# Performance work log

Measured on AMD Instinct MI355X. Metric: run time of the kernel, lower is better.

The kernel has to match this reference:

```python
import jax, jax.numpy as jnp
import numpy as np

H1, W1 = 16, 16  # SparseAttBlock stride
EPS = 1e-5       # BatchNorm eps


def _att(x, wx, bx, wy, by, wo, bo, gamma, beta):
    """DotProductAttBlock: 1x1 q/k projections, full softmax attention over
    the H*W tokens of each (small) block, then 1x1 conv + BatchNorm(train) + ReLU."""
    B, C, H, W = x.shape
    xf = x.reshape(B, C, H * W)                                  # [B,C,N]
    theta = jnp.einsum('mc,bcn->bnm', wx, xf) + bx               # [B,N,fmid]
    psi = jnp.einsum('mc,bcn->bmn', wy, xf) + by[:, None]        # [B,fmid,N]
    alpha = jax.nn.softmax(jnp.einsum('bnm,bmk->bnk', theta, psi), axis=2)  # [B,N,N]
    agg = jnp.einsum('bnk,bck->bcn', alpha, xf)                  # [B,C,N]
    out = jnp.einsum('oc,bcn->bon', wo, agg) + bo[:, None]       # [B,fout,N]
    # BatchNorm2d in training mode: biased batch stats over (batch, spatial)
    mean = out.mean(axis=(0, 2), keepdims=True)
    var = ((out - mean) ** 2).mean(axis=(0, 2), keepdims=True)
    out = (out - mean) * jax.lax.rsqrt(var + EPS) * gamma[:, None] + beta[:, None]
    return jax.nn.relu(out).reshape(B, -1, H, W)


def _forward(x, p1, p2):
    B, C, H, W = x.shape
    h2, w2 = H // H1, W // W1
    # pass 1: attention within each (H1,W1) block, blocks folded into batch
    xb = x.reshape(B, C, H1, h2, W1, w2).transpose(0, 3, 5, 1, 2, 4)
    xb = xb.reshape(B * h2 * w2, C, H1, W1)
    xb = _att(xb, *p1)
    # pass 2: attention across the (h2,w2) block grid
    xb = xb.reshape(B, h2, w2, C, H1, W1).transpose(0, 4, 5, 3, 1, 2)
    xb = xb.reshape(B * H1 * W1, C, h2, w2)
    xb = _att(xb, *p2)
    return xb.reshape(B, H1, W1, C, h2, w2).transpose(0, 3, 1, 4, 2, 5).reshape(B, C, H, W)


def setup_inputs() -> dict:
    key = jax.random.key(0)
    ks = jax.random.split(key, 20)
    B, C, FMID, H, W = 4, 128, 64, 256, 256
    s = 0.05
    d = {'x': jax.random.normal(ks[0], (B, C, H, W), jnp.float32)}
    d['w1x'] = jax.random.normal(ks[1], (FMID, C), jnp.float32) * s
    d['b1x'] = jax.random.normal(ks[2], (FMID,), jnp.float32) * s
    d['w1y'] = jax.random.normal(ks[3], (FMID, C), jnp.float32) * s
    d['b1y'] = jax.random.normal(ks[4], (FMID,), jnp.float32) * s
    d['w1o'] = jax.random.normal(ks[5], (C, C), jnp.float32) * s
    d['b1o'] = jax.random.normal(ks[6], (C,), jnp.float32) * s
    d['g1'] = jnp.ones((C,), jnp.float32)
    d['be1'] = jnp.zeros((C,), jnp.float32)
    d['w2x'] = jax.random.normal(ks[7], (FMID, C), jnp.float32) * s
    d['b2x'] = jax.random.normal(ks[8], (FMID,), jnp.float32) * s
    d['w2y'] = jax.random.normal(ks[9], (FMID, C), jnp.float32) * s
    d['b2y'] = jax.random.normal(ks[10], (FMID,), jnp.float32) * s
    d['w2o'] = jax.random.normal(ks[11], (C, C), jnp.float32) * s
    d['b2o'] = jax.random.normal(ks[12], (C,), jnp.float32) * s
    d['g2'] = jnp.ones((C,), jnp.float32)
    d['be2'] = jnp.zeros((C,), jnp.float32)
    return d


def reference(x, w1x, b1x, w1y, b1y, w1o, b1o, g1, be1,
              w2x, b2x, w2y, b2y, w2o, b2o, g2, be2):
    p1 = (w1x, b1x, w1y, b1y, w1o, b1o, g1, be1)
    p2 = (w2x, b2x, w2y, b2y, w2o, b2o, g2, be2)
    return _forward(x, p1, p2)
```

## Files before the change

### kernel.cpp

```cpp
#include <hip/hip_runtime.h>

typedef _Float16 f16;
typedef f16 f16x2 __attribute__((ext_vector_type(2)));
typedef f16 f16x4 __attribute__((ext_vector_type(4)));
typedef f16 f16x8 __attribute__((ext_vector_type(8)));
typedef float f32x4 __attribute__((ext_vector_type(4)));
typedef float f32x16 __attribute__((ext_vector_type(16)));
typedef unsigned int u32;
typedef u32 u32x2 __attribute__((ext_vector_type(2)));
typedef u32 u32x4 __attribute__((ext_vector_type(4)));

#define MFMA32(a, b, c) __builtin_amdgcn_mfma_f32_32x32x16_f16((a), (b), (c), 0, 0, 0)

__device__ __forceinline__ u32 pk2(float a, float b) {
    return __builtin_bit_cast(u32, __builtin_amdgcn_cvt_pkrtz(a, b));
}
__device__ __forceinline__ f16x4 lo4(f16x8 v) { return __builtin_shufflevector(v, v, 0, 1, 2, 3); }
__device__ __forceinline__ f16x4 hi4(f16x8 v) { return __builtin_shufflevector(v, v, 4, 5, 6, 7); }

__device__ __forceinline__ f16x8 xfrm(f32x16 v, int rb) {
    u32 a0 = pk2(v[rb + 0], v[rb + 1]);
    u32 a1 = pk2(v[rb + 2], v[rb + 3]);
    u32 b0 = pk2(v[rb + 4], v[rb + 5]);
    u32 b1 = pk2(v[rb + 6], v[rb + 7]);
    u32x2 r0 = __builtin_amdgcn_permlane32_swap(a0, b0, false, false);
    u32x2 r1 = __builtin_amdgcn_permlane32_swap(a1, b1, false, false);
    u32x4 aw = {r0.x, r1.x, r0.y, r1.y};
    return __builtin_bit_cast(f16x8, aw);
}
__device__ __forceinline__ f16x8 add8(f16x8 a, f16x8 b) {
    f16x8 r;
#pragma unroll
    for (int j = 0; j < 8; ++j) r[j] = a[j] + b[j];
    return r;
}

#define OFF_Y   65536
#define OFF_SST 98304
#define LDS_ATT 99328

#define WSTRIDE 32896

__global__ __launch_bounds__(512) void repack_kernel(const float* __restrict__ x,
                                                     f16* __restrict__ Xall) {
    __shared__ f16 XT[128 * 264];
    const int tid = threadIdx.x, g = blockIdx.x;
    const int b = g >> 8, i1 = (g >> 4) & 15, i2 = g & 15;
    const int h = i1 * 16 + i2;
    {
        const int c = tid >> 2, wq = (tid & 3) * 64;
        const float* src = x + (((size_t)b * 128 + c) * 256 + h) * 256 + wq;
        f16* dst = XT + c * 264 + wq;
#pragma unroll
        for (int i = 0; i < 16; ++i) {
            f32x4 v = *(const f32x4*)(src + i * 4);
            f16x4 o = {(f16)v[0], (f16)v[1], (f16)v[2], (f16)v[3]};
            *(f16x4*)(dst + i * 4) = o;
        }
    }
    __syncthreads();
    {
        const int w = tid >> 1, ch = (tid & 1) * 64;
        const int j1 = w >> 4, j2 = w & 15;
        f16* dst = Xall + (((size_t)b * 256 + i2 * 16 + j2) * 256 + i1 * 16 + j1) * 128 + ch;
#pragma unroll
        for (int i = 0; i < 8; ++i) {
            f16x8 v;
#pragma unroll
            for (int j = 0; j < 8; ++j) v[j] = XT[(ch + i * 8 + j) * 264 + w];
            *(f16x8*)(dst + i * 8) = v;
        }
    }
}

__global__ void wconv_kernel(const float* __restrict__ w1x, const float* __restrict__ w1y,
                             const float* __restrict__ w1o, const float* __restrict__ b1x,
                             const float* __restrict__ b1y, const float* __restrict__ w2x,
                             const float* __restrict__ w2y, const float* __restrict__ w2o,
                             const float* __restrict__ b2x, const float* __restrict__ b2y,
                             f16* __restrict__ Wf) {
    int i = blockIdx.x * 256 + threadIdx.x;
    if (i < 65536) {
        int p = i >> 15, idx = i & 32767;
        int j = idx & 7, lane = (idx >> 3) & 63, ks = (idx >> 9) & 7, r = idx >> 12;
        int row = r * 32 + (lane & 31);
        int c = ks * 16 + (lane >> 5) * 8 + j;
        const float* s;
        if (p == 0) s = (row < 128) ? w1o + row * 128 : (row < 192) ? w1x + (row - 128) * 128
                                                                   : w1y + (row - 192) * 128;
        else        s = (row < 128) ? w2o + row * 128 : (row < 192) ? w2x + (row - 128) * 128
                                                                   : w2y + (row - 192) * 128;
        Wf[p * WSTRIDE + idx] = (f16)s[c];
    } else {
        int idx2 = i - 65536;
        int p = idx2 >> 7, r = idx2 & 127;
        const float* bsrc = (p == 0) ? ((r < 64) ? b1x : b1y) : ((r < 64) ? b2x : b2y);
        Wf[p * WSTRIDE + 32768 + r] = (f16)bsrc[r & 63];
    }
}

template <int PASS>
__global__ __launch_bounds__(512, 2) void att_kernel(
    const f16* __restrict__ Xin, const f16* __restrict__ Wf, const float* __restrict__ bo,
    const float* __restrict__ bnab, f16* __restrict__ Uout, float* __restrict__ gstats,
    int t_stride, int s_stride) {
    __shared__ __align__(16) char smem[LDS_ATT];
    float* SST = (float*)(smem + OFF_SST);
    const int tid = threadIdx.x;
    const int w = tid >> 6, l = tid & 63, hl = l >> 5, l31 = l & 31;
    const int g = blockIdx.x, R0 = w * 32;

    if (tid < 256) SST[tid] = 0.f;

#pragma unroll
    for (int j = 0; j < 8; ++j) {
        int byte = (j * 512 + tid) * 16;
        *(f16x8*)(smem + byte) = *(const f16x8*)((const char*)Wf + byte);
    }

    const f16* src = Xin + (size_t)g * 32768 + (R0 + l31) * 128 + hl * 8;
    f16x8 afr[8];
#pragma unroll
    for (int ks = 0; ks < 8; ++ks) afr[ks] = *(const f16x8*)(src + ks * 16);
    if constexpr (PASS == 2) {
#pragma unroll
        for (int ks = 0; ks < 8; ++ks) {
            const int c0 = ks * 16 + hl * 8;
            f32x4 a0 = *(const f32x4*)(bnab + c0), a1 = *(const f32x4*)(bnab + c0 + 4);
            f32x4 s0 = *(const f32x4*)(bnab + 128 + c0), s1 = *(const f32x4*)(bnab + 132 + c0);
            f16x8 v = afr[ks];
#pragma unroll
            for (int j = 0; j < 4; ++j) {
                v[j]     = (f16)fmaxf(a0[j] * (float)v[j]     + s0[j], 0.f);
                v[j + 4] = (f16)fmaxf(a1[j] * (float)v[j + 4] + s1[j], 0.f);
            }
            afr[ks] = v;
        }
    }

    const f16* bf = Wf + 32768;
    f16x8 bqf[4], bkf[4];
#pragma unroll
    for (int ks = 0; ks < 4; ++ks) {
        bqf[ks] = *(const f16x8*)(bf + ks * 16 + hl * 8);
        bkf[ks] = *(const f16x8*)(bf + 64 + ks * 16 + hl * 8);
    }
    __syncthreads();

    {
        f32x16 aP[2] = {};
#pragma unroll
        for (int ks = 0; ks < 8; ++ks)
#pragma unroll
            for (int mt = 0; mt < 2; ++mt) {
                f16x8 wk = *(const f16x8*)(smem + (((6 + mt) * 8 + ks) * 64 + l) * 16);
                aP[mt] = MFMA32(wk, afr[ks], aP[mt]);
            }
#pragma unroll
        for (int ks = 0; ks < 4; ++ks) {
            f16x8 yf = add8(xfrm(aP[ks >> 1], 8 * (ks & 1)), bkf[ks]);
            *(f16x8*)(smem + OFF_Y + ((w * 4 + ks) * 64 + l) * 16) = yf;
        }
    }

    f16x8 tb[4];
    {
        f32x16 aT[2] = {};
#pragma unroll
        for (int ks = 0; ks < 8; ++ks)
#pragma unroll
            for (int mt = 0; mt < 2; ++mt) {
                f16x8 wq = *(const f16x8*)(smem + (((4 + mt) * 8 + ks) * 64 + l) * 16);
                aT[mt] = MFMA32(wq, afr[ks], aT[mt]);
            }
#pragma unroll
        for (int ks = 0; ks < 4; ++ks)
            tb[ks] = add8(xfrm(aT[ks >> 1], 8 * (ks & 1)), bqf[ks]);
    }

    f32x16 aV[4] = {};
#pragma unroll
    for (int ks = 0; ks < 8; ++ks)
#pragma unroll
        for (int ct = 0; ct < 4; ++ct) {
            f16x8 wo = *(const f16x8*)(smem + ((ct * 8 + ks) * 64 + l) * 16);
            aV[ct] = MFMA32(afr[ks], wo, aV[ct]);
        }
#pragma unroll
    for (int ct = 0; ct < 4; ++ct) {
        float bov = bo[ct * 32 + l31];
#pragma unroll
        for (int e = 0; e < 16; ++e) aV[ct][e] += bov;
    }
    __syncthreads();

#pragma unroll
    for (int ct = 0; ct < 4; ++ct)
#pragma unroll
        for (int ksl = 0; ksl < 2; ++ksl)
            *(f16x8*)(smem + (((2 * w + ksl) * 4 + ct) * 64 + l) * 16) = xfrm(aV[ct], 8 * ksl);
    __syncthreads();

    f32x16 s[8] = {};
    __builtin_amdgcn_s_setprio(1);
#pragma unroll
    for (int kt = 0; kt < 8; ++kt)
#pragma unroll
        for (int ks = 0; ks < 4; ++ks) {
            f16x8 ay = *(const f16x8*)(smem + OFF_Y + ((kt * 4 + ks) * 64 + l) * 16);
            s[kt] = MFMA32(ay, tb[ks], s[kt]);
        }
    __builtin_amdgcn_s_setprio(0);

    float mx = -1e30f;
#pragma unroll
    for (int kt = 0; kt < 8; ++kt) {
        float m0 = fmaxf(fmaxf(s[kt][0], s[kt][1]), fmaxf(s[kt][2], s[kt][3]));
        float m1 = fmaxf(fmaxf(s[kt][4], s[kt][5]), fmaxf(s[kt][6], s[kt][7]));
        float m2 = fmaxf(fmaxf(s[kt][8], s[kt][9]), fmaxf(s[kt][10], s[kt][11]));
        float m3 = fmaxf(fmaxf(s[kt][12], s[kt][13]), fmaxf(s[kt][14], s[kt][15]));
        mx = fmaxf(mx, fmaxf(fmaxf(m0, m1), fmaxf(m2, m3)));
    }
    mx = fmaxf(mx, __shfl_xor(mx, 32));
    float sum = 0.f;
#pragma unroll
    for (int kt = 0; kt < 8; ++kt)
#pragma unroll
        for (int e = 0; e < 16; ++e) {
            float p = __expf(s[kt][e] - mx);
            s[kt][e] = p;
            sum += p;
        }
    sum += __shfl_xor(sum, 32);
    const float rs = 1.f / sum;
#pragma unroll
    for (int kt = 0; kt < 8; ++kt)
#pragma unroll
        for (int e = 0; e < 16; ++e) s[kt][e] *= rs;

    f32x16 o[4] = {};
#pragma unroll
    for (int kt = 0; kt < 8; ++kt)
#pragma unroll
        for (int ks2 = 0; ks2 < 2; ++ks2) {
            f16x8 ap = xfrm(s[kt], 8 * ks2);
            __builtin_amdgcn_s_setprio(1);
#pragma unroll
            for (int ct = 0; ct < 4; ++ct) {
                f16x8 bv = *(const f16x8*)(smem + (((kt * 2 + ks2) * 4 + ct) * 64 + l) * 16);
                o[ct] = MFMA32(ap, bv, o[ct]);
            }
            __builtin_amdgcn_s_setprio(0);
        }

#pragma unroll
    for (int ct = 0; ct < 4; ++ct) {
        float ss = 0.f, sq = 0.f;
#pragma unroll
        for (int e = 0; e < 16; ++e) {
            float v = o[ct][e];
            ss += v;
            sq += v * v;
        }
        ss += __shfl_xor(ss, 32);
        sq += __shfl_xor(sq, 32);
        if (hl == 0) {
            atomicAdd(&SST[ct * 32 + l31], ss);
            atomicAdd(&SST[128 + ct * 32 + l31], sq);
        }
    }

    const size_t ub = (size_t)(g >> 8) * 8388608 + (size_t)(g & 255) * (size_t)s_stride;
#pragma unroll
    for (int r = 0; r < 16; ++r) {
        int trow = (r & 3) + 8 * (r >> 2) + 4 * hl;
        f16* rp = Uout + ub + (size_t)(R0 + trow) * (size_t)t_stride + l31;
#pragma unroll
        for (int ct = 0; ct < 4; ++ct) rp[ct * 32] = (f16)o[ct][r];
    }
    __syncthreads();
    if (tid < 256) atomicAdd(&gstats[tid], SST[tid]);
}

__global__ void bnfix_kernel(const float* __restrict__ gstats, const float* __restrict__ gamma,
                             const float* __restrict__ beta, float* __restrict__ ab) {
    int c = threadIdx.x;
    if (c < 128) {
        const float inv = 1.f / 262144.f;
        float mean = gstats[c] * inv;
        float var = gstats[128 + c] * inv - mean * mean;
        float rstd = rsqrtf(var + 1e-5f);
        float a = gamma[c] * rstd;
        ab[c] = a;
        ab[128 + c] = beta[c] - mean * a;
    }
}

__global__ __launch_bounds__(256) void final_kernel(const f16* __restrict__ U2,
                                                    const float* __restrict__ ab,
                                                    float* __restrict__ out) {
    __shared__ f16 L[256 * 132];
    const int tid = threadIdx.x, g = blockIdx.x;
    const int b = g >> 8, i1 = (g >> 4) & 15, j1 = g & 15;
    const f16* src = U2 + (size_t)g * 32768;
#pragma unroll
    for (int e = 0; e < 16; ++e) {
        int u = e * 2048 + tid * 8;
        int row = u >> 7, c0 = u & 127;
        f16x8 v = *(const f16x8*)(src + u);
        f16* dst = L + row * 132 + c0;
        *(f16x4*)dst = lo4(v);
        *(f16x4*)(dst + 4) = hi4(v);
    }
    __syncthreads();
    const int j2 = tid & 15, bu = tid >> 4;
#pragma unroll 4
    for (int k = 0; k < 128; ++k) {
        int unit = bu + k * 16;
        int c = unit & 127, i2 = unit >> 7;
        float a = ab[c], bb = ab[128 + c];
        float v = fmaxf(a * (float)L[(i2 * 16 + j2) * 132 + c] + bb, 0.f);
        out[(((size_t)b * 128 + c) * 256 + i1 * 16 + i2) * 256 + j1 * 16 + j2] = v;
    }
}

extern "C" void kernel_launch(void* const* d_in, const int* in_sizes, int n_in, void* d_out,
                              int out_size, void* d_ws, size_t ws_size, hipStream_t stream) {
    (void)in_sizes; (void)n_in; (void)out_size; (void)ws_size;
    const float* x = (const float*)d_in[0];
    const float* w1x = (const float*)d_in[1];
    const float* b1x = (const float*)d_in[2];
    const float* w1y = (const float*)d_in[3];
    const float* b1y = (const float*)d_in[4];
    const float* w1o = (const float*)d_in[5];
    const float* b1o = (const float*)d_in[6];
    const float* g1 = (const float*)d_in[7];
    const float* be1 = (const float*)d_in[8];
    const float* w2x = (const float*)d_in[9];
    const float* b2x = (const float*)d_in[10];
    const float* w2y = (const float*)d_in[11];
    const float* b2y = (const float*)d_in[12];
    const float* w2o = (const float*)d_in[13];
    const float* b2o = (const float*)d_in[14];
    const float* g2 = (const float*)d_in[15];
    const float* be2 = (const float*)d_in[16];

    f16* Xall = (f16*)d_out;
    f16* U1 = (f16*)((char*)d_out + 67108864);
    f16* U2 = (f16*)d_ws;
    f16* Wbf = (f16*)((char*)d_ws + 67108864);
    float* gstats = (float*)((char*)d_ws + 67108864 + 262144);
    float* bnab = gstats + 512;

    (void)hipMemsetAsync(gstats, 0, 2048, stream);
    wconv_kernel<<<257, 256, 0, stream>>>(w1x, w1y, w1o, b1x, b1y, w2x, w2y, w2o, b2x, b2y, Wbf);
    repack_kernel<<<1024, 512, 0, stream>>>(x, Xall);

    att_kernel<1><<<1024, 512, 0, stream>>>(Xall, Wbf, b1o, (const float*)nullptr, U1, gstats,
                                            32768, 128);
    bnfix_kernel<<<1, 128, 0, stream>>>(gstats, g1, be1, bnab);
    att_kernel<2><<<1024, 512, 0, stream>>>(U1, Wbf + WSTRIDE, b2o, bnab, U2, gstats + 256, 128,
                                            32768);
    bnfix_kernel<<<1, 128, 0, stream>>>(gstats + 256, g2, be2, bnab + 256);
    final_kernel<<<1024, 256, 0, stream>>>(U2, bnab + 256, (float*)d_out);
}
```

Baseline: 271.8 us.

## Split fused attention kernel into projection and attention kernels via global scratch

```diff
diff --git a/kernel.cpp b/kernel.cpp
--- a/kernel.cpp
+++ b/kernel.cpp
@@ -100,6 +100,201 @@
 }
 
 template <int PASS>
+__global__ __launch_bounds__(512, 4) void proj_kernel(
+    const f16* Xin, const f16* __restrict__ Wf, const float* __restrict__ bo,
+    const float* __restrict__ bnab, f16* TP, f16* __restrict__ Vf) {
+    const int tid = threadIdx.x, l = tid & 63, hl = l >> 5, l31 = l & 31;
+    const int tt = tid >> 6, g = blockIdx.x;
+
+    const f16* src = Xin + (size_t)g * 32768 + (tt * 32 + l31) * 128 + hl * 8;
+    f16x8 afr[8];
+#pragma unroll
+    for (int ks = 0; ks < 8; ++ks) afr[ks] = *(const f16x8*)(src + ks * 16);
+    if constexpr (PASS == 1) __syncthreads();
+    if constexpr (PASS == 2) {
+#pragma unroll
+        for (int ks = 0; ks < 8; ++ks) {
+            const int c0 = ks * 16 + hl * 8;
+            f32x4 a0 = *(const f32x4*)(bnab + c0), a1 = *(const f32x4*)(bnab + c0 + 4);
+            f32x4 s0 = *(const f32x4*)(bnab + 128 + c0), s1 = *(const f32x4*)(bnab + 132 + c0);
+            f16x8 v = afr[ks];
+#pragma unroll
+            for (int j = 0; j < 4; ++j) {
+                v[j]     = (f16)fmaxf(a0[j] * (float)v[j]     + s0[j], 0.f);
+                v[j + 4] = (f16)fmaxf(a1[j] * (float)v[j + 4] + s1[j], 0.f);
+            }
+            afr[ks] = v;
+        }
+    }
+
+    const f16* bfp = Wf + 32768;
+    f16x8 bqf[4], bkf[4];
+#pragma unroll
+    for (int ks = 0; ks < 4; ++ks) {
+        bqf[ks] = *(const f16x8*)(bfp + ks * 16 + hl * 8);
+        bkf[ks] = *(const f16x8*)(bfp + 64 + ks * 16 + hl * 8);
+    }
+
+    f16* tpg = TP + (size_t)g * 32768;
+
+    {
+        f32x16 aT[2] = {};
+#pragma unroll
+        for (int ks = 0; ks < 8; ++ks) {
+            f16x8 wq0 = *(const f16x8*)(Wf + ((32 + ks) * 64 + l) * 8);
+            f16x8 wq1 = *(const f16x8*)(Wf + ((40 + ks) * 64 + l) * 8);
+            aT[0] = MFMA32(wq0, afr[ks], aT[0]);
+            aT[1] = MFMA32(wq1, afr[ks], aT[1]);
+        }
+#pragma unroll
+        for (int ks = 0; ks < 4; ++ks)
+            *(f16x8*)(tpg + (tt * 4 + ks) * 512 + l * 8) =
+                add8(xfrm(aT[ks >> 1], 8 * (ks & 1)), bqf[ks]);
+    }
+
+    {
+        f32x16 aP[2] = {};
+#pragma unroll
+        for (int ks = 0; ks < 8; ++ks) {
+            f16x8 wk0 = *(const f16x8*)(Wf + ((48 + ks) * 64 + l) * 8);
+            f16x8 wk1 = *(const f16x8*)(Wf + ((56 + ks) * 64 + l) * 8);
+            aP[0] = MFMA32(wk0, afr[ks], aP[0]);
+            aP[1] = MFMA32(wk1, afr[ks], aP[1]);
+        }
+#pragma unroll
+        for (int ks = 0; ks < 4; ++ks)
+            *(f16x8*)(tpg + 16384 + (tt * 4 + ks) * 512 + l * 8) =
+                add8(xfrm(aP[ks >> 1], 8 * (ks & 1)), bkf[ks]);
+    }
+
+    f16* vfg = Vf + (size_t)g * 32768;
+#pragma unroll
+    for (int ch = 0; ch < 2; ++ch) {
+        f32x16 aV[2] = {};
+#pragma unroll
+        for (int ks = 0; ks < 8; ++ks) {
+            f16x8 wo0 = *(const f16x8*)(Wf + (((ch * 2 + 0) * 8 + ks) * 64 + l) * 8);
+            f16x8 wo1 = *(const f16x8*)(Wf + (((ch * 2 + 1) * 8 + ks) * 64 + l) * 8);
+            aV[0] = MFMA32(afr[ks], wo0, aV[0]);
+            aV[1] = MFMA32(afr[ks], wo1, aV[1]);
+        }
+#pragma unroll
+        for (int cc = 0; cc < 2; ++cc) {
+            const int ct = ch * 2 + cc;
+            float bov = bo[ct * 32 + l31];
+#pragma unroll
+            for (int e = 0; e < 16; ++e) aV[cc][e] += bov;
+#pragma unroll
+            for (int ksl = 0; ksl < 2; ++ksl)
+                *(f16x8*)(vfg + (2 * tt + ksl) * 2048 + ct * 512 + l * 8) = xfrm(aV[cc], 8 * ksl);
+        }
+    }
+}
+
+template <int PASS>
+__global__ __launch_bounds__(256, 2) void attn_kernel(
+    const f16* __restrict__ TP, const f16* __restrict__ Vf, f16* __restrict__ Uout,
+    float* __restrict__ gstats, int t_stride, int s_stride) {
+    __shared__ float SST[256];
+    const int tid = threadIdx.x, l = tid & 63, hl = l >> 5, l31 = l & 31;
+    const int bid = blockIdx.x;
+    const int g = (bid >> 4) * 8 + (bid & 7);
+    const int tt = ((bid >> 3) & 1) * 4 + (tid >> 6);
+    const int R0 = tt * 32;
+
+    SST[tid] = 0.f;
+    __syncthreads();
+
+    const f16* tpg = TP + (size_t)g * 32768;
+
+    f16x8 tb[4];
+#pragma unroll
+    for (int ks = 0; ks < 4; ++ks)
+        tb[ks] = *(const f16x8*)(tpg + (tt * 4 + ks) * 512 + l * 8);
+
+    f32x16 s[8] = {};
+    __builtin_amdgcn_s_setprio(1);
+#pragma unroll
+    for (int kt = 0; kt < 8; ++kt)
+#pragma unroll
+        for (int ks = 0; ks < 4; ++ks) {
+            f16x8 ay = *(const f16x8*)(tpg + 16384 + (kt * 4 + ks) * 512 + l * 8);
+            s[kt] = MFMA32(ay, tb[ks], s[kt]);
+        }
+    __builtin_amdgcn_s_setprio(0);
+
+    float mx = -1e30f;
+#pragma unroll
+    for (int kt = 0; kt < 8; ++kt) {
+        float m0 = fmaxf(fmaxf(s[kt][0], s[kt][1]), fmaxf(s[kt][2], s[kt][3]));
+        float m1 = fmaxf(fmaxf(s[kt][4], s[kt][5]), fmaxf(s[kt][6], s[kt][7]));
+        float m2 = fmaxf(fmaxf(s[kt][8], s[kt][9]), fmaxf(s[kt][10], s[kt][11]));
+        float m3 = fmaxf(fmaxf(s[kt][12], s[kt][13]), fmaxf(s[kt][14], s[kt][15]));
+        mx = fmaxf(mx, fmaxf(fmaxf(m0, m1), fmaxf(m2, m3)));
+    }
+    mx = fmaxf(mx, __shfl_xor(mx, 32));
+    float sum = 0.f;
+#pragma unroll
+    for (int kt = 0; kt < 8; ++kt)
+#pragma unroll
+        for (int e = 0; e < 16; ++e) {
+            float p = __expf(s[kt][e] - mx);
+            s[kt][e] = p;
+            sum += p;
+        }
+    sum += __shfl_xor(sum, 32);
+    const float rs = 1.f / sum;
+#pragma unroll
+    for (int kt = 0; kt < 8; ++kt)
+#pragma unroll
+        for (int e = 0; e < 16; ++e) s[kt][e] *= rs;
+
+    const f16* vfg = Vf + (size_t)g * 32768;
+    f32x16 o[4] = {};
+#pragma unroll
+    for (int kt = 0; kt < 8; ++kt)
+#pragma unroll
+        for (int ks2 = 0; ks2 < 2; ++ks2) {
+            f16x8 ap = xfrm(s[kt], 8 * ks2);
+            __builtin_amdgcn_s_setprio(1);
+#pragma unroll
+            for (int ct = 0; ct < 4; ++ct) {
+                f16x8 bv = *(const f16x8*)(vfg + ((kt * 2 + ks2) * 2048 + ct * 512 + l * 8));
+                o[ct] = MFMA32(ap, bv, o[ct]);
+            }
+            __builtin_amdgcn_s_setprio(0);
+        }
+
+#pragma unroll
+    for (int ct = 0; ct < 4; ++ct) {
+        float ss = 0.f, sq = 0.f;
+#pragma unroll
+        for (int e = 0; e < 16; ++e) {
+            float v = o[ct][e];
+            ss += v;
+            sq += v * v;
+        }
+        ss += __shfl_xor(ss, 32);
+        sq += __shfl_xor(sq, 32);
+        if (hl == 0) {
+            atomicAdd(&SST[ct * 32 + l31], ss);
+            atomicAdd(&SST[128 + ct * 32 + l31], sq);
+        }
+    }
+
+    const size_t ub = (size_t)(g >> 8) * 8388608 + (size_t)(g & 255) * (size_t)s_stride;
+#pragma unroll
+    for (int r = 0; r < 16; ++r) {
+        int trow = (r & 3) + 8 * (r >> 2) + 4 * hl;
+        f16* rp = Uout + ub + (size_t)(R0 + trow) * (size_t)t_stride + l31;
+#pragma unroll
+        for (int ct = 0; ct < 4; ++ct) rp[ct * 32] = (f16)o[ct][r];
+    }
+    __syncthreads();
+    atomicAdd(&gstats[tid], SST[tid]);
+}
+
+template <int PASS>
 __global__ __launch_bounds__(512, 2) void att_kernel(
     const f16* __restrict__ Xin, const f16* __restrict__ Wf, const float* __restrict__ bo,
     const float* __restrict__ bnab, f16* __restrict__ Uout, float* __restrict__ gstats,
@@ -138,12 +333,12 @@
         }
     }
 
-    const f16* bf = Wf + 32768;
+    const f16* bfp = Wf + 32768;
     f16x8 bqf[4], bkf[4];
 #pragma unroll
     for (int ks = 0; ks < 4; ++ks) {
-        bqf[ks] = *(const f16x8*)(bf + ks * 16 + hl * 8);
-        bkf[ks] = *(const f16x8*)(bf + 64 + ks * 16 + hl * 8);
+        bqf[ks] = *(const f16x8*)(bfp + ks * 16 + hl * 8);
+        bkf[ks] = *(const f16x8*)(bfp + 64 + ks * 16 + hl * 8);
     }
     __syncthreads();
 
@@ -326,7 +521,7 @@
 
 extern "C" void kernel_launch(void* const* d_in, const int* in_sizes, int n_in, void* d_out,
                               int out_size, void* d_ws, size_t ws_size, hipStream_t stream) {
-    (void)in_sizes; (void)n_in; (void)out_size; (void)ws_size;
+    (void)in_sizes; (void)n_in; (void)out_size;
     const float* x = (const float*)d_in[0];
     const float* w1x = (const float*)d_in[1];
     const float* b1x = (const float*)d_in[2];
@@ -347,20 +542,46 @@
 
     f16* Xall = (f16*)d_out;
     f16* U1 = (f16*)((char*)d_out + 67108864);
-    f16* U2 = (f16*)d_ws;
-    f16* Wbf = (f16*)((char*)d_ws + 67108864);
-    float* gstats = (float*)((char*)d_ws + 67108864 + 262144);
-    float* bnab = gstats + 512;
-
-    (void)hipMemsetAsync(gstats, 0, 2048, stream);
-    wconv_kernel<<<257, 256, 0, stream>>>(w1x, w1y, w1o, b1x, b1y, w2x, w2y, w2o, b2x, b2y, Wbf);
-    repack_kernel<<<1024, 512, 0, stream>>>(x, Xall);
-
-    att_kernel<1><<<1024, 512, 0, stream>>>(Xall, Wbf, b1o, (const float*)nullptr, U1, gstats,
-                                            32768, 128);
-    bnfix_kernel<<<1, 128, 0, stream>>>(gstats, g1, be1, bnab);
-    att_kernel<2><<<1024, 512, 0, stream>>>(U1, Wbf + WSTRIDE, b2o, bnab, U2, gstats + 256, 128,
-                                            32768);
-    bnfix_kernel<<<1, 128, 0, stream>>>(gstats + 256, g2, be2, bnab + 256);
-    final_kernel<<<1024, 256, 0, stream>>>(U2, bnab + 256, (float*)d_out);
-}
+
+    if (ws_size >= (size_t)134500000) {
+        f16* TP = (f16*)d_out;
+        f16* Vfp = (f16*)d_ws;
+        f16* U2 = (f16*)((char*)d_ws + 67108864);
+        f16* Wbf = (f16*)((char*)d_ws + 134217728);
+        float* gstats = (float*)((char*)d_ws + 134217728 + 131584);
+        float* bnab = gstats + 512;
+
+        (void)hipMemsetAsync(gstats, 0, 2048, stream);
+        wconv_kernel<<<257, 256, 0, stream>>>(w1x, w1y, w1o, b1x, b1y, w2x, w2y, w2o, b2x, b2y,
+                                              Wbf);
+        repack_kernel<<<1024, 512, 0, stream>>>(x, Xall);
+
+        proj_kernel<1><<<1024, 512, 0, stream>>>(Xall, Wbf, b1o, (const float*)nullptr, TP, Vfp);
+        attn_kernel<1><<<2048, 256, 0, stream>>>(TP, Vfp, U1, gstats, 32768, 128);
+        bnfix_kernel<<<1, 128, 0, stream>>>(gstats, g1, be1, bnab);
+
+        proj_kernel<2><<<1024, 512, 0, stream>>>(U1, Wbf + WSTRIDE, b2o, bnab, TP, Vfp);
+        attn_kernel<2><<<2048, 256, 0, stream>>>(TP, Vfp, U2, gstats + 256, 128, 32768);
+        bnfix_kernel<<<1, 128, 0, stream>>>(gstats + 256, g2, be2, bnab + 256);
+
+        final_kernel<<<1024, 256, 0, stream>>>(U2, bnab + 256, (float*)d_out);
+    } else {
+        f16* U2 = (f16*)d_ws;
+        f16* Wbf = (f16*)((char*)d_ws + 67108864);
+        float* gstats = (float*)((char*)d_ws + 67108864 + 262144);
+        float* bnab = gstats + 512;
+
+        (void)hipMemsetAsync(gstats, 0, 2048, stream);
+        wconv_kernel<<<257, 256, 0, stream>>>(w1x, w1y, w1o, b1x, b1y, w2x, w2y, w2o, b2x, b2y,
+                                              Wbf);
+        repack_kernel<<<1024, 512, 0, stream>>>(x, Xall);
+
+        att_kernel<1><<<1024, 512, 0, stream>>>(Xall, Wbf, b1o, (const float*)nullptr, U1, gstats,
+                                                32768, 128);
+        bnfix_kernel<<<1, 128, 0, stream>>>(gstats, g1, be1, bnab);
+        att_kernel<2><<<1024, 512, 0, stream>>>(U1, Wbf + WSTRIDE, b2o, bnab, U2, gstats + 256,
+                                                128, 32768);
+        bnfix_kernel<<<1, 128, 0, stream>>>(gstats + 256, g2, be2, bnab + 256);
+        final_kernel<<<1024, 256, 0, stream>>>(U2, bnab + 256, (float*)d_out);
+    }
+}
```

Result: slower. 416.4 us (+53.2%).

## Make attention kernels persistent over four tiles with register-accumulated BN stats

Applied to the files above, without the earlier changes.

```diff
diff --git a/kernel.cpp b/kernel.cpp
--- a/kernel.cpp
+++ b/kernel.cpp
@@ -36,8 +36,8 @@
 }
 
 #define OFF_Y   65536
-#define OFF_SST 98304
-#define LDS_ATT 99328
+#define OFF_V   98304
+#define LDS_ATT 163840
 
 #define WSTRIDE 32896
 
@@ -105,181 +105,207 @@
     const float* __restrict__ bnab, f16* __restrict__ Uout, float* __restrict__ gstats,
     int t_stride, int s_stride) {
     __shared__ __align__(16) char smem[LDS_ATT];
-    float* SST = (float*)(smem + OFF_SST);
     const int tid = threadIdx.x;
     const int w = tid >> 6, l = tid & 63, hl = l >> 5, l31 = l & 31;
-    const int g = blockIdx.x, R0 = w * 32;
-
-    if (tid < 256) SST[tid] = 0.f;
-
-#pragma unroll
-    for (int j = 0; j < 8; ++j) {
-        int byte = (j * 512 + tid) * 16;
-        *(f16x8*)(smem + byte) = *(const f16x8*)((const char*)Wf + byte);
-    }
-
-    const f16* src = Xin + (size_t)g * 32768 + (R0 + l31) * 128 + hl * 8;
-    f16x8 afr[8];
-#pragma unroll
-    for (int ks = 0; ks < 8; ++ks) afr[ks] = *(const f16x8*)(src + ks * 16);
-    if constexpr (PASS == 2) {
-#pragma unroll
-        for (int ks = 0; ks < 8; ++ks) {
-            const int c0 = ks * 16 + hl * 8;
-            f32x4 a0 = *(const f32x4*)(bnab + c0), a1 = *(const f32x4*)(bnab + c0 + 4);
-            f32x4 s0 = *(const f32x4*)(bnab + 128 + c0), s1 = *(const f32x4*)(bnab + 132 + c0);
-            f16x8 v = afr[ks];
-#pragma unroll
-            for (int j = 0; j < 4; ++j) {
-                v[j]     = (f16)fmaxf(a0[j] * (float)v[j]     + s0[j], 0.f);
-                v[j + 4] = (f16)fmaxf(a1[j] * (float)v[j + 4] + s1[j], 0.f);
-            }
-            afr[ks] = v;
-        }
-    }
-
-    const f16* bf = Wf + 32768;
+    const int R0 = w * 32;
+
+    const f16* bfp = Wf + 32768;
     f16x8 bqf[4], bkf[4];
 #pragma unroll
     for (int ks = 0; ks < 4; ++ks) {
-        bqf[ks] = *(const f16x8*)(bf + ks * 16 + hl * 8);
-        bkf[ks] = *(const f16x8*)(bf + 64 + ks * 16 + hl * 8);
+        bqf[ks] = *(const f16x8*)(bfp + ks * 16 + hl * 8);
+        bkf[ks] = *(const f16x8*)(bfp + 64 + ks * 16 + hl * 8);
+    }
+    float bov[4];
+#pragma unroll
+    for (int ct = 0; ct < 4; ++ct) bov[ct] = bo[ct * 32 + l31];
+    float ssa[4] = {0.f, 0.f, 0.f, 0.f}, sqa[4] = {0.f, 0.f, 0.f, 0.f};
+
+    {
+        f16x8 wv[8];
+#pragma unroll
+        for (int j = 0; j < 8; ++j)
+            wv[j] = *(const f16x8*)((const char*)Wf + (j * 512 + tid) * 16);
+#pragma unroll
+        for (int j = 0; j < 8; ++j)
+            *(f16x8*)(smem + (j * 512 + tid) * 16) = wv[j];
     }
     __syncthreads();
 
-    {
-        f32x16 aP[2] = {};
-#pragma unroll
-        for (int ks = 0; ks < 8; ++ks)
-#pragma unroll
-            for (int mt = 0; mt < 2; ++mt) {
-                f16x8 wk = *(const f16x8*)(smem + (((6 + mt) * 8 + ks) * 64 + l) * 16);
-                aP[mt] = MFMA32(wk, afr[ks], aP[mt]);
-            }
-#pragma unroll
-        for (int ks = 0; ks < 4; ++ks) {
-            f16x8 yf = add8(xfrm(aP[ks >> 1], 8 * (ks & 1)), bkf[ks]);
-            *(f16x8*)(smem + OFF_Y + ((w * 4 + ks) * 64 + l) * 16) = yf;
-        }
-    }
-
-    f16x8 tb[4];
-    {
-        f32x16 aT[2] = {};
-#pragma unroll
-        for (int ks = 0; ks < 8; ++ks)
-#pragma unroll
-            for (int mt = 0; mt < 2; ++mt) {
-                f16x8 wq = *(const f16x8*)(smem + (((4 + mt) * 8 + ks) * 64 + l) * 16);
-                aT[mt] = MFMA32(wq, afr[ks], aT[mt]);
-            }
-#pragma unroll
-        for (int ks = 0; ks < 4; ++ks)
-            tb[ks] = add8(xfrm(aT[ks >> 1], 8 * (ks & 1)), bqf[ks]);
-    }
-
-    f32x16 aV[4] = {};
-#pragma unroll
-    for (int ks = 0; ks < 8; ++ks)
+    for (int it = 0; it < 4; ++it) {
+        const int g = blockIdx.x + it * 256;
+
+        f16x8 afr[8];
+        {
+            const f16* src = Xin + (size_t)g * 32768 + (R0 + l31) * 128 + hl * 8;
+#pragma unroll
+            for (int ks = 0; ks < 8; ++ks) afr[ks] = *(const f16x8*)(src + ks * 16);
+        }
+        if constexpr (PASS == 2) {
+#pragma unroll
+            for (int ks = 0; ks < 8; ++ks) {
+                const int c0 = ks * 16 + hl * 8;
+                f32x4 a0 = *(const f32x4*)(bnab + c0), a1 = *(const f32x4*)(bnab + c0 + 4);
+                f32x4 s0 = *(const f32x4*)(bnab + 128 + c0), s1 = *(const f32x4*)(bnab + 132 + c0);
+                f16x8 v = afr[ks];
+#pragma unroll
+                for (int j = 0; j < 4; ++j) {
+                    v[j]     = (f16)fmaxf(a0[j] * (float)v[j]     + s0[j], 0.f);
+                    v[j + 4] = (f16)fmaxf(a1[j] * (float)v[j + 4] + s1[j], 0.f);
+                }
+                afr[ks] = v;
+            }
+        }
+
+        {
+            f32x16 aP[2] = {};
+#pragma unroll
+            for (int ks = 0; ks < 8; ++ks)
+#pragma unroll
+                for (int mt = 0; mt < 2; ++mt) {
+                    f16x8 wk = *(const f16x8*)(smem + (((6 + mt) * 8 + ks) * 64 + l) * 16);
+                    aP[mt] = MFMA32(wk, afr[ks], aP[mt]);
+                }
+#pragma unroll
+            for (int ks = 0; ks < 4; ++ks) {
+                f16x8 yf = add8(xfrm(aP[ks >> 1], 8 * (ks & 1)), bkf[ks]);
+                *(f16x8*)(smem + OFF_Y + ((w * 4 + ks) * 64 + l) * 16) = yf;
+            }
+        }
+
+        f16x8 tb[4];
+        {
+            f32x16 aT[2] = {};
+#pragma unroll
+            for (int ks = 0; ks < 8; ++ks)
+#pragma unroll
+                for (int mt = 0; mt < 2; ++mt) {
+                    f16x8 wq = *(const f16x8*)(smem + (((4 + mt) * 8 + ks) * 64 + l) * 16);
+                    aT[mt] = MFMA32(wq, afr[ks], aT[mt]);
+                }
+#pragma unroll
+            for (int ks = 0; ks < 4; ++ks)
+                tb[ks] = add8(xfrm(aT[ks >> 1], 8 * (ks & 1)), bqf[ks]);
+        }
+
+        {
+            f32x16 aV[4] = {};
+#pragma unroll
+            for (int ks = 0; ks < 8; ++ks)
+#pragma unroll
+                for (int ct = 0; ct < 4; ++ct) {
+                    f16x8 wo = *(const f16x8*)(smem + ((ct * 8 + ks) * 64 + l) * 16);
+                    aV[ct] = MFMA32(afr[ks], wo, aV[ct]);
+                }
+#pragma unroll
+            for (int ct = 0; ct < 4; ++ct) {
+#pragma unroll
+                for (int e = 0; e < 16; ++e) aV[ct][e] += bov[ct];
+#pragma unroll
+                for (int ksl = 0; ksl < 2; ++ksl)
+                    *(f16x8*)(smem + OFF_V + (((2 * w + ksl) * 4 + ct) * 64 + l) * 16) =
+                        xfrm(aV[ct], 8 * ksl);
+            }
+        }
+        __syncthreads();
+
+        f32x16 s[8] = {};
+        __builtin_amdgcn_s_setprio(1);
+#pragma unroll
+        for (int kt = 0; kt < 8; ++kt)
+#pragma unroll
+            for (int ks = 0; ks < 4; ++ks) {
+                f16x8 ay = *(const f16x8*)(smem + OFF_Y + ((kt * 4 + ks) * 64 + l) * 16);
+                s[kt] = MFMA32(ay, tb[ks], s[kt]);
+            }
+        __builtin_amdgcn_s_setprio(0);
+
+        float mx = -1e30f;
+#pragma unroll
+        for (int kt = 0; kt < 8; ++kt) {
+            float m0 = fmaxf(fmaxf(s[kt][0], s[kt][1]), fmaxf(s[kt][2], s[kt][3]));
+            float m1 = fmaxf(fmaxf(s[kt][4], s[kt][5]), fmaxf(s[kt][6], s[kt][7]));
+            float m2 = fmaxf(fmaxf(s[kt][8], s[kt][9]), fmaxf(s[kt][10], s[kt][11]));
+            float m3 = fmaxf(fmaxf(s[kt][12], s[kt][13]), fmaxf(s[kt][14], s[kt][15]));
+            mx = fmaxf(mx, fmaxf(fmaxf(m0, m1), fmaxf(m2, m3)));
+        }
+        mx = fmaxf(mx, __shfl_xor(mx, 32));
+        float sum = 0.f;
+#pragma unroll
+        for (int kt = 0; kt < 8; ++kt)
+#pragma unroll
+            for (int e = 0; e < 16; ++e) {
+                float p = __expf(s[kt][e] - mx);
+                s[kt][e] = p;
+                sum += p;
+            }
+        sum += __shfl_xor(sum, 32);
+        const float rs = 1.f / sum;
+#pragma unroll
+        for (int kt = 0; kt < 8; ++kt)
+#pragma unroll
+            for (int e = 0; e < 16; ++e) s[kt][e] *= rs;
+
+        f32x16 o[4] = {};
+#pragma unroll
+        for (int kt = 0; kt < 8; ++kt)
+#pragma unroll
+            for (int ks2 = 0; ks2 < 2; ++ks2) {
+                f16x8 ap = xfrm(s[kt], 8 * ks2);
+                __builtin_amdgcn_s_setprio(1);
+#pragma unroll
+                for (int ct = 0; ct < 4; ++ct) {
+                    f16x8 bv =
+                        *(const f16x8*)(smem + OFF_V + (((kt * 2 + ks2) * 4 + ct) * 64 + l) * 16);
+                    o[ct] = MFMA32(ap, bv, o[ct]);
+                }
+                __builtin_amdgcn_s_setprio(0);
+            }
+
+        const size_t ub = (size_t)(g >> 8) * 8388608 + (size_t)(g & 255) * (size_t)s_stride;
 #pragma unroll
         for (int ct = 0; ct < 4; ++ct) {
-            f16x8 wo = *(const f16x8*)(smem + ((ct * 8 + ks) * 64 + l) * 16);
-            aV[ct] = MFMA32(afr[ks], wo, aV[ct]);
-        }
+            float ss = 0.f, sq = 0.f;
+#pragma unroll
+            for (int e = 0; e < 16; ++e) {
+                float v = o[ct][e];
+                ss += v;
+                sq += v * v;
+            }
+            ssa[ct] += ss;
+            sqa[ct] += sq;
+        }
+#pragma unroll
+        for (int r = 0; r < 16; ++r) {
+            int trow = (r & 3) + 8 * (r >> 2) + 4 * hl;
+            f16* rp = Uout + ub + (size_t)(R0 + trow) * (size_t)t_stride + l31;
+#pragma unroll
+            for (int ct = 0; ct < 4; ++ct) rp[ct * 32] = (f16)o[ct][r];
+        }
+        __syncthreads();
+    }
+
 #pragma unroll
     for (int ct = 0; ct < 4; ++ct) {
-        float bov = bo[ct * 32 + l31];
-#pragma unroll
-        for (int e = 0; e < 16; ++e) aV[ct][e] += bov;
+        ssa[ct] += __shfl_xor(ssa[ct], 32);
+        sqa[ct] += __shfl_xor(sqa[ct], 32);
+    }
+    float* SS = (float*)(smem + OFF_Y);
+    if (hl == 0) {
+#pragma unroll
+        for (int ct = 0; ct < 4; ++ct) {
+            SS[w * 128 + ct * 32 + l31] = ssa[ct];
+            SS[1024 + w * 128 + ct * 32 + l31] = sqa[ct];
+        }
     }
     __syncthreads();
-
-#pragma unroll
-    for (int ct = 0; ct < 4; ++ct)
-#pragma unroll
-        for (int ksl = 0; ksl < 2; ++ksl)
-            *(f16x8*)(smem + (((2 * w + ksl) * 4 + ct) * 64 + l) * 16) = xfrm(aV[ct], 8 * ksl);
-    __syncthreads();
-
-    f32x16 s[8] = {};
-    __builtin_amdgcn_s_setprio(1);
-#pragma unroll
-    for (int kt = 0; kt < 8; ++kt)
-#pragma unroll
-        for (int ks = 0; ks < 4; ++ks) {
-            f16x8 ay = *(const f16x8*)(smem + OFF_Y + ((kt * 4 + ks) * 64 + l) * 16);
-            s[kt] = MFMA32(ay, tb[ks], s[kt]);
-        }
-    __builtin_amdgcn_s_setprio(0);
-
-    float mx = -1e30f;
-#pragma unroll
-    for (int kt = 0; kt < 8; ++kt) {
-        float m0 = fmaxf(fmaxf(s[kt][0], s[kt][1]), fmaxf(s[kt][2], s[kt][3]));
-        float m1 = fmaxf(fmaxf(s[kt][4], s[kt][5]), fmaxf(s[kt][6], s[kt][7]));
-        float m2 = fmaxf(fmaxf(s[kt][8], s[kt][9]), fmaxf(s[kt][10], s[kt][11]));
-        float m3 = fmaxf(fmaxf(s[kt][12], s[kt][13]), fmaxf(s[kt][14], s[kt][15]));
-        mx = fmaxf(mx, fmaxf(fmaxf(m0, m1), fmaxf(m2, m3)));
-    }
-    mx = fmaxf(mx, __shfl_xor(mx, 32));
-    float sum = 0.f;
-#pragma unroll
-    for (int kt = 0; kt < 8; ++kt)
-#pragma unroll
-        for (int e = 0; e < 16; ++e) {
-            float p = __expf(s[kt][e] - mx);
-            s[kt][e] = p;
-            sum += p;
-        }
-    sum += __shfl_xor(sum, 32);
-    const float rs = 1.f / sum;
-#pragma unroll
-    for (int kt = 0; kt < 8; ++kt)
-#pragma unroll
-        for (int e = 0; e < 16; ++e) s[kt][e] *= rs;
-
-    f32x16 o[4] = {};
-#pragma unroll
-    for (int kt = 0; kt < 8; ++kt)
-#pragma unroll
-        for (int ks2 = 0; ks2 < 2; ++ks2) {
-            f16x8 ap = xfrm(s[kt], 8 * ks2);
-            __builtin_amdgcn_s_setprio(1);
-#pragma unroll
-            for (int ct = 0; ct < 4; ++ct) {
-                f16x8 bv = *(const f16x8*)(smem + (((kt * 2 + ks2) * 4 + ct) * 64 + l) * 16);
-                o[ct] = MFMA32(ap, bv, o[ct]);
-            }
-            __builtin_amdgcn_s_setprio(0);
-        }
-
-#pragma unroll
-    for (int ct = 0; ct < 4; ++ct) {
-        float ss = 0.f, sq = 0.f;
-#pragma unroll
-        for (int e = 0; e < 16; ++e) {
-            float v = o[ct][e];
-            ss += v;
-            sq += v * v;
-        }
-        ss += __shfl_xor(ss, 32);
-        sq += __shfl_xor(sq, 32);
-        if (hl == 0) {
-            atomicAdd(&SST[ct * 32 + l31], ss);
-            atomicAdd(&SST[128 + ct * 32 + l31], sq);
-        }
-    }
-
-    const size_t ub = (size_t)(g >> 8) * 8388608 + (size_t)(g & 255) * (size_t)s_stride;
-#pragma unroll
-    for (int r = 0; r < 16; ++r) {
-        int trow = (r & 3) + 8 * (r >> 2) + 4 * hl;
-        f16* rp = Uout + ub + (size_t)(R0 + trow) * (size_t)t_stride + l31;
-#pragma unroll
-        for (int ct = 0; ct < 4; ++ct) rp[ct * 32] = (f16)o[ct][r];
-    }
-    __syncthreads();
-    if (tid < 256) atomicAdd(&gstats[tid], SST[tid]);
+    if (tid < 256) {
+        int c = tid & 127, which = tid >> 7;
+        float acc = 0.f;
+#pragma unroll
+        for (int iw = 0; iw < 8; ++iw) acc += SS[which * 1024 + iw * 128 + c];
+        atomicAdd(&gstats[which * 128 + c], acc);
+    }
 }
 
 __global__ void bnfix_kernel(const float* __restrict__ gstats, const float* __restrict__ gamma,
@@ -356,11 +382,11 @@
     wconv_kernel<<<257, 256, 0, stream>>>(w1x, w1y, w1o, b1x, b1y, w2x, w2y, w2o, b2x, b2y, Wbf);
     repack_kernel<<<1024, 512, 0, stream>>>(x, Xall);
 
-    att_kernel<1><<<1024, 512, 0, stream>>>(Xall, Wbf, b1o, (const float*)nullptr, U1, gstats,
-                                            32768, 128);
+    att_kernel<1><<<256, 512, 0, stream>>>(Xall, Wbf, b1o, (const float*)nullptr, U1, gstats,
+                                           32768, 128);
     bnfix_kernel<<<1, 128, 0, stream>>>(gstats, g1, be1, bnab);
-    att_kernel<2><<<1024, 512, 0, stream>>>(U1, Wbf + WSTRIDE, b2o, bnab, U2, gstats + 256, 128,
-                                            32768);
+    att_kernel<2><<<256, 512, 0, stream>>>(U1, Wbf + WSTRIDE, b2o, bnab, U2, gstats + 256, 128,
+                                           32768);
     bnfix_kernel<<<1, 128, 0, stream>>>(gstats + 256, g2, be2, bnab + 256);
     final_kernel<<<1024, 256, 0, stream>>>(U2, bnab + 256, (float*)d_out);
 }
```

Result: slower. 333.2 us (+22.6%).
